# Performance work log

Measured on AMD Instinct MI355X. Metric: run time of the kernel, lower is better.

The kernel has to match this reference:

```python
import jax, jax.numpy as jnp
import numpy as np

D = 500  # hidden width hard-coded in the module

def _lrelu(x):
    # nn.LeakyReLU default negative_slope = 0.01
    return jnp.where(x > 0, x, 0.01 * x)

def setup_inputs() -> dict:
    key = jax.random.key(0)
    ks = jax.random.split(key, 20)
    T, B = 2048, 64
    inp = {
        "pitches": jax.random.normal(ks[0], (T, B, 128), dtype=jnp.float32),
        "velocities": jax.random.normal(ks[1], (T, B, 128), dtype=jnp.float32),
        "durations": jax.random.uniform(ks[2], (T, B, 1), dtype=jnp.float32),
        "steps": jax.random.uniform(ks[3], (T, B, 1), dtype=jnp.float32),
        # learned params (torch Linear convention: W is [out, in])
        "Wp": jax.random.normal(ks[4], (D, 128), dtype=jnp.float32) * 0.05,
        "bp": jax.random.normal(ks[5], (D,), dtype=jnp.float32) * 0.05,
        "Wv": jax.random.normal(ks[6], (D, 128), dtype=jnp.float32) * 0.05,
        "bv": jax.random.normal(ks[7], (D,), dtype=jnp.float32) * 0.05,
        "Wd": jax.random.normal(ks[8], (D, 1), dtype=jnp.float32) * 0.05,
        "bd": jax.random.normal(ks[9], (D,), dtype=jnp.float32) * 0.05,
        "Ws": jax.random.normal(ks[10], (D, 1), dtype=jnp.float32) * 0.05,
        "bs": jax.random.normal(ks[11], (D,), dtype=jnp.float32) * 0.05,
        "W1": jax.random.normal(ks[12], (D, D), dtype=jnp.float32) * 0.05,
        "b1": jax.random.normal(ks[13], (D,), dtype=jnp.float32) * 0.05,
        "W2": jax.random.normal(ks[14], (D, D), dtype=jnp.float32) * 0.05,
        "b2": jax.random.normal(ks[15], (D,), dtype=jnp.float32) * 0.05,
        "Wi": jax.random.normal(ks[16], (D, D), dtype=jnp.float32) * 0.05,
        "bi": jax.random.normal(ks[17], (D,), dtype=jnp.float32) * 0.05,
        "W3": jax.random.normal(ks[18], (1, D), dtype=jnp.float32) * 0.05,
        "b3": jax.random.normal(ks[19], (1,), dtype=jnp.float32) * 0.05,
    }
    return inp

def reference(pitches, velocities, durations, steps,
              Wp, bp, Wv, bv, Wd, bd, Ws, bs,
              W1, b1, W2, b2, Wi, bi, W3, b3):
    # Note: in the original torch code the LSTMCell output is computed then
    # discarded (overwritten), and `info` at step t depends only on inputs at
    # step t. Thus the final output depends only on the last timestep through
    # the embed-sum -> LeakyReLU MLP -> linear_intermediate chain.
    # Vectorized over all T timesteps (same per-step math as the loop body).
    add = (jnp.einsum('tbi,oi->tbo', pitches, Wp) + bp
           + jnp.einsum('tbi,oi->tbo', velocities, Wv) + bv
           + jnp.einsum('tbi,oi->tbo', durations, Wd) + bd
           + jnp.einsum('tbi,oi->tbo', steps, Ws) + bs)      # [T,B,500]
    h = _lrelu(jnp.einsum('tbi,oi->tbo', add, W1) + b1)
    h = _lrelu(jnp.einsum('tbi,oi->tbo', h, W2) + b2)
    info = jnp.einsum('tbi,oi->tbo', h, Wi) + bi              # [T,B,500]
    out = jax.nn.sigmoid(info[-1] @ W3.T + b3)                # [B,1]
    return out
```

## Files before the change

kernel.cpp:

```cpp
#include <hip/hip_runtime.h>

#define DD 500
#define BB 64
#define TT 2048
#define KP 128
#define VCHUNKS 32
#define VPSTRIDE 512

__global__ __launch_bounds__(256) void k_embed_v(
    const float* __restrict__ pitches, const float* __restrict__ velocities,
    const float* __restrict__ durations, const float* __restrict__ steps,
    const float* __restrict__ Wp, const float* __restrict__ bp,
    const float* __restrict__ Wv, const float* __restrict__ bv,
    const float* __restrict__ Wd, const float* __restrict__ bd,
    const float* __restrict__ Wst, const float* __restrict__ bs,
    const float* __restrict__ Wi, const float* __restrict__ W3,
    const float* __restrict__ W1, const float* __restrict__ W2,
    float* __restrict__ addT, float* __restrict__ vpart,
    float* __restrict__ dummy)
{
    const int tid = threadIdx.x;
    const int bid = blockIdx.x;

    if (bid >= 157) {
        const int pb = bid - 157;
        const int slice = pb >> 3;
        const float4* W1f = (const float4*)W1;
        const float4* W2f = (const float4*)W2;
        float acc = 0.f;
        const int jend = (slice + 1) * 15625;
        for (int j = slice * 15625 + tid; j < jend; j += 256) {
            float4 p = (j < 62500) ? W1f[j] : W2f[j - 62500];
            acc += p.x + p.y + p.z + p.w;
        }
        dummy[bid] = acc;
        return;
    }

    if (bid >= 125) {
        const int oc = bid - 125;
        const int obeg = oc * 16;
        const int k0 = tid;
        const int k1 = tid + 256;
        float acc0 = 0.f, acc1 = 0.f;
        #pragma unroll
        for (int i = 0; i < 16; ++i) {
            const int o = obeg + i;
            const int oc_ = o < DD ? o : DD - 1;
            const float w = o < DD ? W3[oc_] : 0.f;
            acc0 += w * Wi[(size_t)oc_ * DD + k0];
            if (k1 < DD) acc1 += w * Wi[(size_t)oc_ * DD + k1];
        }
        vpart[oc * VPSTRIDE + k0] = acc0;
        if (k1 < DD) vpart[oc * VPSTRIDE + k1] = acc1;
        return;
    }

    __shared__ float lds[KP * BB];
    const int b = tid & 63;
    const int o = __builtin_amdgcn_readfirstlane(bid * 4 + (tid >> 6));
    const float* __restrict__ wp = Wp + o * KP;
    const float* __restrict__ wv = Wv + o * KP;

    float a0 = 0.f, a1 = 0.f, a2 = 0.f, a3 = 0.f;

    const float4* Psrc = (const float4*)(pitches + (size_t)(TT - 1) * BB * KP);
    const float4* Vsrc = (const float4*)(velocities + (size_t)(TT - 1) * BB * KP);

    for (int j = tid; j < BB * KP / 4; j += 256) {
        float4 p = Psrc[j];
        int pb = j >> 5;
        int k0 = (j & 31) * 4;
        lds[(k0 + 0) * BB + ((pb + k0 + 0) & 63)] = p.x;
        lds[(k0 + 1) * BB + ((pb + k0 + 1) & 63)] = p.y;
        lds[(k0 + 2) * BB + ((pb + k0 + 2) & 63)] = p.z;
        lds[(k0 + 3) * BB + ((pb + k0 + 3) & 63)] = p.w;
    }
    __syncthreads();
    for (int k = 0; k < KP; k += 4) {
        a0 += lds[(k + 0) * BB + ((b + k + 0) & 63)] * wp[k + 0];
        a1 += lds[(k + 1) * BB + ((b + k + 1) & 63)] * wp[k + 1];
        a2 += lds[(k + 2) * BB + ((b + k + 2) & 63)] * wp[k + 2];
        a3 += lds[(k + 3) * BB + ((b + k + 3) & 63)] * wp[k + 3];
    }
    __syncthreads();

    for (int j = tid; j < BB * KP / 4; j += 256) {
        float4 p = Vsrc[j];
        int pb = j >> 5;
        int k0 = (j & 31) * 4;
        lds[(k0 + 0) * BB + ((pb + k0 + 0) & 63)] = p.x;
        lds[(k0 + 1) * BB + ((pb + k0 + 1) & 63)] = p.y;
        lds[(k0 + 2) * BB + ((pb + k0 + 2) & 63)] = p.z;
        lds[(k0 + 3) * BB + ((pb + k0 + 3) & 63)] = p.w;
    }
    __syncthreads();
    for (int k = 0; k < KP; k += 4) {
        a0 += lds[(k + 0) * BB + ((b + k + 0) & 63)] * wv[k + 0];
        a1 += lds[(k + 1) * BB + ((b + k + 1) & 63)] * wv[k + 1];
        a2 += lds[(k + 2) * BB + ((b + k + 2) & 63)] * wv[k + 2];
        a3 += lds[(k + 3) * BB + ((b + k + 3) & 63)] * wv[k + 3];
    }

    const float dur = durations[(size_t)(TT - 1) * BB + b];
    const float st  = steps[(size_t)(TT - 1) * BB + b];
    const float acc = bp[o] + bv[o] + bd[o] + bs[o]
                    + dur * Wd[o] + st * Wst[o]
                    + (a0 + a1) + (a2 + a3);
    addT[o * BB + b] = acc;
}

__global__ __launch_bounds__(256) void k_dense(
    const float* __restrict__ Ain, const float* __restrict__ W,
    const float* __restrict__ bias, float* __restrict__ Aout, int leaky)
{
    __shared__ float partial[4][BB];
    const int tid = threadIdx.x;
    const int b = tid & 63;
    const int w = tid >> 6;
    const int o = blockIdx.x;
    const float* __restrict__ wrow = W + o * DD;
    const int kbeg = w * 125;

    float a0 = 0.f, a1 = 0.f, a2 = 0.f, a3 = 0.f;
    float a4 = 0.f, a5 = 0.f, a6 = 0.f, a7 = 0.f;
    #pragma unroll 3
    for (int k = kbeg; k < kbeg + 120; k += 8) {
        a0 += Ain[(k + 0) * BB + b] * wrow[k + 0];
        a1 += Ain[(k + 1) * BB + b] * wrow[k + 1];
        a2 += Ain[(k + 2) * BB + b] * wrow[k + 2];
        a3 += Ain[(k + 3) * BB + b] * wrow[k + 3];
        a4 += Ain[(k + 4) * BB + b] * wrow[k + 4];
        a5 += Ain[(k + 5) * BB + b] * wrow[k + 5];
        a6 += Ain[(k + 6) * BB + b] * wrow[k + 6];
        a7 += Ain[(k + 7) * BB + b] * wrow[k + 7];
    }
    {
        const int k = kbeg + 120;
        a0 += Ain[(k + 0) * BB + b] * wrow[k + 0];
        a1 += Ain[(k + 1) * BB + b] * wrow[k + 1];
        a2 += Ain[(k + 2) * BB + b] * wrow[k + 2];
        a3 += Ain[(k + 3) * BB + b] * wrow[k + 3];
        a4 += Ain[(k + 4) * BB + b] * wrow[k + 4];
    }
    partial[w][b] = ((a0 + a1) + (a2 + a3)) + ((a4 + a5) + (a6 + a7));
    __syncthreads();
    if (w == 0) {
        float acc = bias[o] + (partial[0][b] + partial[1][b])
                            + (partial[2][b] + partial[3][b]);
        if (leaky) acc = acc > 0.f ? acc : 0.01f * acc;
        Aout[o * BB + b] = acc;
    }
}

__global__ __launch_bounds__(256) void k_out(
    const float* __restrict__ h2T, const float* __restrict__ vpart,
    const float* __restrict__ W3, const float* __restrict__ bi,
    const float* __restrict__ b3, float* __restrict__ out)
{
    __shared__ float vv[DD];
    __shared__ float partial[4][BB];
    const int tid = threadIdx.x;

    for (int k = tid; k < DD; k += 256) {
        float s0 = 0.f, s1 = 0.f, s2 = 0.f, s3 = 0.f;
        float s4 = 0.f, s5 = 0.f, s6 = 0.f, s7 = 0.f;
        #pragma unroll
        for (int oc = 0; oc < VCHUNKS; oc += 8) {
            s0 += vpart[(oc + 0) * VPSTRIDE + k];
            s1 += vpart[(oc + 1) * VPSTRIDE + k];
            s2 += vpart[(oc + 2) * VPSTRIDE + k];
            s3 += vpart[(oc + 3) * VPSTRIDE + k];
            s4 += vpart[(oc + 4) * VPSTRIDE + k];
            s5 += vpart[(oc + 5) * VPSTRIDE + k];
            s6 += vpart[(oc + 6) * VPSTRIDE + k];
            s7 += vpart[(oc + 7) * VPSTRIDE + k];
        }
        vv[k] = ((s0 + s1) + (s2 + s3)) + ((s4 + s5) + (s6 + s7));
    }
    __syncthreads();

    const int b = tid & 63;
    const int w = tid >> 6;
    const int kbeg = w * 125;

    float accA = 0.f, accB = 0.f;
    for (int k = kbeg; k < kbeg + 125; ++k) {
        accA += h2T[k * BB + b] * vv[k];
        accB += W3[k] * bi[k];
    }
    partial[w][b] = accA + accB;
    __syncthreads();
    if (w == 0) {
        float s = partial[0][b] + partial[1][b] + partial[2][b] + partial[3][b]
                + b3[0];
        out[b] = 1.f / (1.f + __expf(-s));
    }
}

extern "C" void kernel_launch(void* const* d_in, const int* in_sizes, int n_in,
                              void* d_out, int out_size, void* d_ws, size_t ws_size,
                              hipStream_t stream)
{
    const float* pitches    = (const float*)d_in[0];
    const float* velocities = (const float*)d_in[1];
    const float* durations  = (const float*)d_in[2];
    const float* steps      = (const float*)d_in[3];
    const float* Wp  = (const float*)d_in[4];
    const float* bp  = (const float*)d_in[5];
    const float* Wv  = (const float*)d_in[6];
    const float* bv  = (const float*)d_in[7];
    const float* Wd  = (const float*)d_in[8];
    const float* bd  = (const float*)d_in[9];
    const float* Wst = (const float*)d_in[10];
    const float* bs  = (const float*)d_in[11];
    const float* W1  = (const float*)d_in[12];
    const float* b1  = (const float*)d_in[13];
    const float* W2  = (const float*)d_in[14];
    const float* b2  = (const float*)d_in[15];
    const float* Wi  = (const float*)d_in[16];
    const float* bi  = (const float*)d_in[17];
    const float* W3  = (const float*)d_in[18];
    const float* b3  = (const float*)d_in[19];

    float* ws    = (float*)d_ws;
    float* addT  = ws;
    float* h1T   = ws + 32000;
    float* h2T   = ws + 64000;
    float* vpart = ws + 96000;
    float* dummy = ws + 96000 + VCHUNKS * VPSTRIDE;

    float* out = (float*)d_out;

    k_embed_v<<<221, 256, 0, stream>>>(pitches, velocities, durations, steps,
                                       Wp, bp, Wv, bv, Wd, bd, Wst, bs,
                                       Wi, W3, W1, W2, addT, vpart, dummy);
    k_dense<<<500, 256, 0, stream>>>(addT, W1, b1, h1T, 1);
    k_dense<<<500, 256, 0, stream>>>(h1T, W2, b2, h2T, 1);
    k_out<<<1, 256, 0, stream>>>(h2T, vpart, W3, bi, b3, out);
}
```

Before: 220.6 us.

## Fuse embed, two dense layers and output into one flag-synchronized persistent kernel

Replaces the four kernel launches with a single 500-block kernel. Stages are chained through per-block magic-value flags in the workspace, polled with agent-scope atomic loads and s_sleep, so launch gaps and inter-kernel drains go away. It also drops the dummy pass that read W1/W2 ahead of time. The flags are never reset between calls, so on repeated launches later stages can read h1T/h2T before the current call has written them. Progress also depends on all 500 blocks being resident at the same time.

```diff
diff --git a/kernel.cpp b/kernel.cpp
--- a/kernel.cpp
+++ b/kernel.cpp
@@ -6,8 +6,21 @@
 #define KP 128
 #define VCHUNKS 32
 #define VPSTRIDE 512
-
-__global__ __launch_bounds__(256) void k_embed_v(
+#define NBLK 500
+
+#define MAGIC_A 0x51A6E001
+#define MAGIC_V 0x51A6E002
+#define MAGIC_B 0x51A6E003
+#define MAGIC_C 0x51A6E004
+
+__device__ __forceinline__ int agent_load(const int* p) {
+    return __hip_atomic_load(p, __ATOMIC_RELAXED, __HIP_MEMORY_SCOPE_AGENT);
+}
+__device__ __forceinline__ void agent_store(int* p, int v) {
+    __hip_atomic_store(p, v, __ATOMIC_RELAXED, __HIP_MEMORY_SCOPE_AGENT);
+}
+
+__global__ __launch_bounds__(256, 2) void k_fused(
     const float* __restrict__ pitches, const float* __restrict__ velocities,
     const float* __restrict__ durations, const float* __restrict__ steps,
     const float* __restrict__ Wp, const float* __restrict__ bp,
@@ -15,29 +28,76 @@
     const float* __restrict__ Wd, const float* __restrict__ bd,
     const float* __restrict__ Wst, const float* __restrict__ bs,
     const float* __restrict__ Wi, const float* __restrict__ W3,
-    const float* __restrict__ W1, const float* __restrict__ W2,
-    float* __restrict__ addT, float* __restrict__ vpart,
-    float* __restrict__ dummy)
+    const float* __restrict__ W1, const float* __restrict__ b1,
+    const float* __restrict__ W2, const float* __restrict__ b2,
+    const float* __restrict__ bi, const float* __restrict__ b3,
+    float* __restrict__ addT, float* __restrict__ h1T,
+    float* __restrict__ h2T, float* __restrict__ vpart,
+    int* __restrict__ flagA, int* __restrict__ flagB,
+    int* __restrict__ flagC, int* __restrict__ flagV,
+    float* __restrict__ out)
 {
+    __shared__ float lds[KP * BB];
+    __shared__ float partial[4][BB];
+    __shared__ float vv[DD];
+
     const int tid = threadIdx.x;
     const int bid = blockIdx.x;
-
-    if (bid >= 157) {
-        const int pb = bid - 157;
-        const int slice = pb >> 3;
-        const float4* W1f = (const float4*)W1;
-        const float4* W2f = (const float4*)W2;
-        float acc = 0.f;
-        const int jend = (slice + 1) * 15625;
-        for (int j = slice * 15625 + tid; j < jend; j += 256) {
-            float4 p = (j < 62500) ? W1f[j] : W2f[j - 62500];
-            acc += p.x + p.y + p.z + p.w;
-        }
-        dummy[bid] = acc;
-        return;
-    }
-
-    if (bid >= 125) {
+    const int b = tid & 63;
+    const int w = tid >> 6;
+
+    if (bid < 125) {
+        const int o = __builtin_amdgcn_readfirstlane(bid * 4 + w);
+        const float* __restrict__ wp = Wp + o * KP;
+        const float* __restrict__ wvv = Wv + o * KP;
+        float a0 = 0.f, a1 = 0.f, a2 = 0.f, a3 = 0.f;
+
+        const float4* Psrc = (const float4*)(pitches + (size_t)(TT - 1) * BB * KP);
+        const float4* Vsrc = (const float4*)(velocities + (size_t)(TT - 1) * BB * KP);
+
+        for (int j = tid; j < BB * KP / 4; j += 256) {
+            float4 p = Psrc[j];
+            int pb = j >> 5;
+            int k0 = (j & 31) * 4;
+            lds[(k0 + 0) * BB + ((pb + k0 + 0) & 63)] = p.x;
+            lds[(k0 + 1) * BB + ((pb + k0 + 1) & 63)] = p.y;
+            lds[(k0 + 2) * BB + ((pb + k0 + 2) & 63)] = p.z;
+            lds[(k0 + 3) * BB + ((pb + k0 + 3) & 63)] = p.w;
+        }
+        __syncthreads();
+        for (int k = 0; k < KP; k += 4) {
+            a0 += lds[(k + 0) * BB + ((b + k + 0) & 63)] * wp[k + 0];
+            a1 += lds[(k + 1) * BB + ((b + k + 1) & 63)] * wp[k + 1];
+            a2 += lds[(k + 2) * BB + ((b + k + 2) & 63)] * wp[k + 2];
+            a3 += lds[(k + 3) * BB + ((b + k + 3) & 63)] * wp[k + 3];
+        }
+        __syncthreads();
+        for (int j = tid; j < BB * KP / 4; j += 256) {
+            float4 p = Vsrc[j];
+            int pb = j >> 5;
+            int k0 = (j & 31) * 4;
+            lds[(k0 + 0) * BB + ((pb + k0 + 0) & 63)] = p.x;
+            lds[(k0 + 1) * BB + ((pb + k0 + 1) & 63)] = p.y;
+            lds[(k0 + 2) * BB + ((pb + k0 + 2) & 63)] = p.z;
+            lds[(k0 + 3) * BB + ((pb + k0 + 3) & 63)] = p.w;
+        }
+        __syncthreads();
+        for (int k = 0; k < KP; k += 4) {
+            a0 += lds[(k + 0) * BB + ((b + k + 0) & 63)] * wvv[k + 0];
+            a1 += lds[(k + 1) * BB + ((b + k + 1) & 63)] * wvv[k + 1];
+            a2 += lds[(k + 2) * BB + ((b + k + 2) & 63)] * wvv[k + 2];
+            a3 += lds[(k + 3) * BB + ((b + k + 3) & 63)] * wvv[k + 3];
+        }
+
+        const float dur = durations[(size_t)(TT - 1) * BB + b];
+        const float st  = steps[(size_t)(TT - 1) * BB + b];
+        addT[o * BB + b] = bp[o] + bv[o] + bd[o] + bs[o]
+                         + dur * Wd[o] + st * Wst[o]
+                         + (a0 + a1) + (a2 + a3);
+        __threadfence();
+        __syncthreads();
+        if (tid == 0) agent_store(&flagA[bid], MAGIC_A);
+    } else if (bid < 157) {
         const int oc = bid - 125;
         const int obeg = oc * 16;
         const int k0 = tid;
@@ -47,120 +107,113 @@
         for (int i = 0; i < 16; ++i) {
             const int o = obeg + i;
             const int oc_ = o < DD ? o : DD - 1;
-            const float w = o < DD ? W3[oc_] : 0.f;
-            acc0 += w * Wi[(size_t)oc_ * DD + k0];
-            if (k1 < DD) acc1 += w * Wi[(size_t)oc_ * DD + k1];
+            const float ww = o < DD ? W3[oc_] : 0.f;
+            acc0 += ww * Wi[(size_t)oc_ * DD + k0];
+            if (k1 < DD) acc1 += ww * Wi[(size_t)oc_ * DD + k1];
         }
         vpart[oc * VPSTRIDE + k0] = acc0;
         if (k1 < DD) vpart[oc * VPSTRIDE + k1] = acc1;
-        return;
-    }
-
-    __shared__ float lds[KP * BB];
-    const int b = tid & 63;
-    const int o = __builtin_amdgcn_readfirstlane(bid * 4 + (tid >> 6));
-    const float* __restrict__ wp = Wp + o * KP;
-    const float* __restrict__ wv = Wv + o * KP;
-
-    float a0 = 0.f, a1 = 0.f, a2 = 0.f, a3 = 0.f;
-
-    const float4* Psrc = (const float4*)(pitches + (size_t)(TT - 1) * BB * KP);
-    const float4* Vsrc = (const float4*)(velocities + (size_t)(TT - 1) * BB * KP);
-
-    for (int j = tid; j < BB * KP / 4; j += 256) {
-        float4 p = Psrc[j];
-        int pb = j >> 5;
-        int k0 = (j & 31) * 4;
-        lds[(k0 + 0) * BB + ((pb + k0 + 0) & 63)] = p.x;
-        lds[(k0 + 1) * BB + ((pb + k0 + 1) & 63)] = p.y;
-        lds[(k0 + 2) * BB + ((pb + k0 + 2) & 63)] = p.z;
-        lds[(k0 + 3) * BB + ((pb + k0 + 3) & 63)] = p.w;
-    }
-    __syncthreads();
-    for (int k = 0; k < KP; k += 4) {
-        a0 += lds[(k + 0) * BB + ((b + k + 0) & 63)] * wp[k + 0];
-        a1 += lds[(k + 1) * BB + ((b + k + 1) & 63)] * wp[k + 1];
-        a2 += lds[(k + 2) * BB + ((b + k + 2) & 63)] * wp[k + 2];
-        a3 += lds[(k + 3) * BB + ((b + k + 3) & 63)] * wp[k + 3];
-    }
-    __syncthreads();
-
-    for (int j = tid; j < BB * KP / 4; j += 256) {
-        float4 p = Vsrc[j];
-        int pb = j >> 5;
-        int k0 = (j & 31) * 4;
-        lds[(k0 + 0) * BB + ((pb + k0 + 0) & 63)] = p.x;
-        lds[(k0 + 1) * BB + ((pb + k0 + 1) & 63)] = p.y;
-        lds[(k0 + 2) * BB + ((pb + k0 + 2) & 63)] = p.z;
-        lds[(k0 + 3) * BB + ((pb + k0 + 3) & 63)] = p.w;
-    }
-    __syncthreads();
-    for (int k = 0; k < KP; k += 4) {
-        a0 += lds[(k + 0) * BB + ((b + k + 0) & 63)] * wv[k + 0];
-        a1 += lds[(k + 1) * BB + ((b + k + 1) & 63)] * wv[k + 1];
-        a2 += lds[(k + 2) * BB + ((b + k + 2) & 63)] * wv[k + 2];
-        a3 += lds[(k + 3) * BB + ((b + k + 3) & 63)] * wv[k + 3];
-    }
-
-    const float dur = durations[(size_t)(TT - 1) * BB + b];
-    const float st  = steps[(size_t)(TT - 1) * BB + b];
-    const float acc = bp[o] + bv[o] + bd[o] + bs[o]
-                    + dur * Wd[o] + st * Wst[o]
-                    + (a0 + a1) + (a2 + a3);
-    addT[o * BB + b] = acc;
-}
-
-__global__ __launch_bounds__(256) void k_dense(
-    const float* __restrict__ Ain, const float* __restrict__ W,
-    const float* __restrict__ bias, float* __restrict__ Aout, int leaky)
-{
-    __shared__ float partial[4][BB];
-    const int tid = threadIdx.x;
-    const int b = tid & 63;
-    const int w = tid >> 6;
-    const int o = blockIdx.x;
-    const float* __restrict__ wrow = W + o * DD;
-    const int kbeg = w * 125;
-
-    float a0 = 0.f, a1 = 0.f, a2 = 0.f, a3 = 0.f;
-    float a4 = 0.f, a5 = 0.f, a6 = 0.f, a7 = 0.f;
-    #pragma unroll 3
-    for (int k = kbeg; k < kbeg + 120; k += 8) {
-        a0 += Ain[(k + 0) * BB + b] * wrow[k + 0];
-        a1 += Ain[(k + 1) * BB + b] * wrow[k + 1];
-        a2 += Ain[(k + 2) * BB + b] * wrow[k + 2];
-        a3 += Ain[(k + 3) * BB + b] * wrow[k + 3];
-        a4 += Ain[(k + 4) * BB + b] * wrow[k + 4];
-        a5 += Ain[(k + 5) * BB + b] * wrow[k + 5];
-        a6 += Ain[(k + 6) * BB + b] * wrow[k + 6];
-        a7 += Ain[(k + 7) * BB + b] * wrow[k + 7];
-    }
+        __threadfence();
+        __syncthreads();
+        if (tid == 0) agent_store(&flagV[oc], MAGIC_V);
+    }
+
+    if (tid < 125) {
+        while (agent_load(&flagA[tid]) != MAGIC_A) __builtin_amdgcn_s_sleep(1);
+    }
+    __threadfence();
+    __syncthreads();
+
     {
-        const int k = kbeg + 120;
-        a0 += Ain[(k + 0) * BB + b] * wrow[k + 0];
-        a1 += Ain[(k + 1) * BB + b] * wrow[k + 1];
-        a2 += Ain[(k + 2) * BB + b] * wrow[k + 2];
-        a3 += Ain[(k + 3) * BB + b] * wrow[k + 3];
-        a4 += Ain[(k + 4) * BB + b] * wrow[k + 4];
-    }
-    partial[w][b] = ((a0 + a1) + (a2 + a3)) + ((a4 + a5) + (a6 + a7));
-    __syncthreads();
-    if (w == 0) {
-        float acc = bias[o] + (partial[0][b] + partial[1][b])
-                            + (partial[2][b] + partial[3][b]);
-        if (leaky) acc = acc > 0.f ? acc : 0.01f * acc;
-        Aout[o * BB + b] = acc;
-    }
-}
-
-__global__ __launch_bounds__(256) void k_out(
-    const float* __restrict__ h2T, const float* __restrict__ vpart,
-    const float* __restrict__ W3, const float* __restrict__ bi,
-    const float* __restrict__ b3, float* __restrict__ out)
-{
-    __shared__ float vv[DD];
-    __shared__ float partial[4][BB];
-    const int tid = threadIdx.x;
+        const float* __restrict__ wrow = W1 + bid * DD;
+        const int kbeg = w * 125;
+        float a0 = 0.f, a1 = 0.f, a2 = 0.f, a3 = 0.f;
+        float a4 = 0.f, a5 = 0.f, a6 = 0.f, a7 = 0.f;
+        #pragma unroll 3
+        for (int k = kbeg; k < kbeg + 120; k += 8) {
+            a0 += addT[(k + 0) * BB + b] * wrow[k + 0];
+            a1 += addT[(k + 1) * BB + b] * wrow[k + 1];
+            a2 += addT[(k + 2) * BB + b] * wrow[k + 2];
+            a3 += addT[(k + 3) * BB + b] * wrow[k + 3];
+            a4 += addT[(k + 4) * BB + b] * wrow[k + 4];
+            a5 += addT[(k + 5) * BB + b] * wrow[k + 5];
+            a6 += addT[(k + 6) * BB + b] * wrow[k + 6];
+            a7 += addT[(k + 7) * BB + b] * wrow[k + 7];
+        }
+        {
+            const int k = kbeg + 120;
+            a0 += addT[(k + 0) * BB + b] * wrow[k + 0];
+            a1 += addT[(k + 1) * BB + b] * wrow[k + 1];
+            a2 += addT[(k + 2) * BB + b] * wrow[k + 2];
+            a3 += addT[(k + 3) * BB + b] * wrow[k + 3];
+            a4 += addT[(k + 4) * BB + b] * wrow[k + 4];
+        }
+        partial[w][b] = ((a0 + a1) + (a2 + a3)) + ((a4 + a5) + (a6 + a7));
+        __syncthreads();
+        if (w == 0) {
+            float acc = b1[bid] + (partial[0][b] + partial[1][b])
+                                + (partial[2][b] + partial[3][b]);
+            acc = acc > 0.f ? acc : 0.01f * acc;
+            h1T[bid * BB + b] = acc;
+            __threadfence();
+        }
+        __syncthreads();
+        if (tid == 0) agent_store(&flagB[bid], MAGIC_B);
+    }
+
+    for (int i = tid; i < NBLK; i += 256) {
+        while (agent_load(&flagB[i]) != MAGIC_B) __builtin_amdgcn_s_sleep(1);
+    }
+    __threadfence();
+    __syncthreads();
+
+    {
+        const float* __restrict__ wrow = W2 + bid * DD;
+        const int kbeg = w * 125;
+        float a0 = 0.f, a1 = 0.f, a2 = 0.f, a3 = 0.f;
+        float a4 = 0.f, a5 = 0.f, a6 = 0.f, a7 = 0.f;
+        #pragma unroll 3
+        for (int k = kbeg; k < kbeg + 120; k += 8) {
+            a0 += h1T[(k + 0) * BB + b] * wrow[k + 0];
+            a1 += h1T[(k + 1) * BB + b] * wrow[k + 1];
+            a2 += h1T[(k + 2) * BB + b] * wrow[k + 2];
+            a3 += h1T[(k + 3) * BB + b] * wrow[k + 3];
+            a4 += h1T[(k + 4) * BB + b] * wrow[k + 4];
+            a5 += h1T[(k + 5) * BB + b] * wrow[k + 5];
+            a6 += h1T[(k + 6) * BB + b] * wrow[k + 6];
+            a7 += h1T[(k + 7) * BB + b] * wrow[k + 7];
+        }
+        {
+            const int k = kbeg + 120;
+            a0 += h1T[(k + 0) * BB + b] * wrow[k + 0];
+            a1 += h1T[(k + 1) * BB + b] * wrow[k + 1];
+            a2 += h1T[(k + 2) * BB + b] * wrow[k + 2];
+            a3 += h1T[(k + 3) * BB + b] * wrow[k + 3];
+            a4 += h1T[(k + 4) * BB + b] * wrow[k + 4];
+        }
+        partial[w][b] = ((a0 + a1) + (a2 + a3)) + ((a4 + a5) + (a6 + a7));
+        __syncthreads();
+        if (w == 0) {
+            float acc = b2[bid] + (partial[0][b] + partial[1][b])
+                                + (partial[2][b] + partial[3][b]);
+            acc = acc > 0.f ? acc : 0.01f * acc;
+            h2T[bid * BB + b] = acc;
+            __threadfence();
+        }
+        __syncthreads();
+        if (tid == 0) agent_store(&flagC[bid], MAGIC_C);
+    }
+
+    if (bid != 0) return;
+
+    for (int i = tid; i < NBLK; i += 256) {
+        while (agent_load(&flagC[i]) != MAGIC_C) __builtin_amdgcn_s_sleep(1);
+    }
+    if (tid < VCHUNKS) {
+        while (agent_load(&flagV[tid]) != MAGIC_V) __builtin_amdgcn_s_sleep(1);
+    }
+    __threadfence();
+    __syncthreads();
 
     for (int k = tid; k < DD; k += 256) {
         float s0 = 0.f, s1 = 0.f, s2 = 0.f, s3 = 0.f;
@@ -180,20 +233,25 @@
     }
     __syncthreads();
 
-    const int b = tid & 63;
-    const int w = tid >> 6;
-    const int kbeg = w * 125;
-
-    float accA = 0.f, accB = 0.f;
-    for (int k = kbeg; k < kbeg + 125; ++k) {
-        accA += h2T[k * BB + b] * vv[k];
-        accB += W3[k] * bi[k];
-    }
-    partial[w][b] = accA + accB;
+    {
+        const int kbeg = w * 125;
+        float p0 = 0.f, p1 = 0.f, p2 = 0.f, p3 = 0.f;
+        for (int k = kbeg; k < kbeg + 124; k += 4) {
+            p0 += h2T[(k + 0) * BB + b] * vv[k + 0] + W3[k + 0] * bi[k + 0];
+            p1 += h2T[(k + 1) * BB + b] * vv[k + 1] + W3[k + 1] * bi[k + 1];
+            p2 += h2T[(k + 2) * BB + b] * vv[k + 2] + W3[k + 2] * bi[k + 2];
+            p3 += h2T[(k + 3) * BB + b] * vv[k + 3] + W3[k + 3] * bi[k + 3];
+        }
+        {
+            const int k = kbeg + 124;
+            p0 += h2T[k * BB + b] * vv[k] + W3[k] * bi[k];
+        }
+        partial[w][b] = (p0 + p1) + (p2 + p3);
+    }
     __syncthreads();
     if (w == 0) {
-        float s = partial[0][b] + partial[1][b] + partial[2][b] + partial[3][b]
-                + b3[0];
+        float s = b3[0] + (partial[0][b] + partial[1][b])
+                        + (partial[2][b] + partial[3][b]);
         out[b] = 1.f / (1.f + __expf(-s));
     }
 }
@@ -228,14 +286,17 @@
     float* h1T   = ws + 32000;
     float* h2T   = ws + 64000;
     float* vpart = ws + 96000;
-    float* dummy = ws + 96000 + VCHUNKS * VPSTRIDE;
+    int*   flags = (int*)(ws + 96000 + VCHUNKS * VPSTRIDE);
+    int*   flagA = flags;
+    int*   flagB = flags + 128;
+    int*   flagC = flags + 640;
+    int*   flagV = flags + 1152;
 
     float* out = (float*)d_out;
 
-    k_embed_v<<<221, 256, 0, stream>>>(pitches, velocities, durations, steps,
-                                       Wp, bp, Wv, bv, Wd, bd, Wst, bs,
-                                       Wi, W3, W1, W2, addT, vpart, dummy);
-    k_dense<<<500, 256, 0, stream>>>(addT, W1, b1, h1T, 1);
-    k_dense<<<500, 256, 0, stream>>>(h1T, W2, b2, h2T, 1);
-    k_out<<<1, 256, 0, stream>>>(h2T, vpart, W3, bi, b3, out);
+    k_fused<<<NBLK, 256, 0, stream>>>(pitches, velocities, durations, steps,
+                                      Wp, bp, Wv, bv, Wd, bd, Wst, bs,
+                                      Wi, W3, W1, b1, W2, b2, bi, b3,
+                                      addT, h1T, h2T, vpart,
+                                      flagA, flagB, flagC, flagV, out);
 }
```

Result: slower. 282.5 us (+28.0%).
